# Kernel tuning notes

Hardware: AMD Instinct MI355X
Metric: run time of the kernel (lower is better)

## Reference

```python
import jax, jax.numpy as jnp
import numpy as np

BETA = 0.5
THRESHOLD = 14.0

def softplus_custom(x):
    # torch.nn.Softplus(beta=0.5, threshold=14): (1/beta)*log1p(exp(beta*x)) if beta*x<=threshold else x
    bx = BETA * x
    return jnp.where(bx > THRESHOLD, x, (1.0 / BETA) * jnp.log1p(jnp.exp(jnp.minimum(bx, THRESHOLD))))

def setup_inputs() -> dict:
    key = jax.random.key(0)
    ks = jax.random.split(key, 12)
    N, E, RBF, D = 50000, 800000, 100, 64
    inp = {
        'rbf': jax.random.normal(ks[0], (E, RBF), dtype=jnp.float32),
        'edge_f': jax.random.normal(ks[1], (E, D), dtype=jnp.float32),
        'new_node': jax.random.normal(ks[2], (N, D), dtype=jnp.float32),
        'W1': jax.random.normal(ks[3], (RBF, D), dtype=jnp.float32) * (1.0 / np.sqrt(RBF)),
        'b1': jax.random.normal(ks[4], (D,), dtype=jnp.float32) * 0.01,
        'W2': jax.random.normal(ks[5], (D, D), dtype=jnp.float32) * (1.0 / np.sqrt(D)),
        'b2': jax.random.normal(ks[6], (D,), dtype=jnp.float32) * 0.01,
        'W3': jax.random.normal(ks[7], (D, D), dtype=jnp.float32) * (1.0 / np.sqrt(D)),
        'b3': jax.random.normal(ks[8], (D,), dtype=jnp.float32) * 0.01,
        'src': jax.random.randint(ks[9], (E,), 0, N, dtype=jnp.int32),
        'dst': jax.random.randint(ks[10], (E,), 0, N, dtype=jnp.int32),
    }
    return inp

def reference(rbf, edge_f, new_node, W1, b1, W2, b2, W3, b3, src, dst):
    N = new_node.shape[0]
    # update_rbf: linear -> softplus(beta=0.5, threshold=14) -> linear, per edge
    h = softplus_custom(rbf @ W1 + b1) @ W2 + b2            # [E, D]
    # update_edge: linear on edge features
    edge_f_new = edge_f @ W3 + b3                            # [E, D]
    # message: u_mul_e (source node feature * edge h) and copy_e; reduce: segmented sum to dst
    msg = new_node[src] * h + edge_f_new                     # [E, D]
    out = jax.ops.segment_sum(msg, dst, num_segments=N)      # [N, D]
    return out
```

## Files before the change

kernel.cpp:

```cpp
#include <hip/hip_runtime.h>

#define RBF_DIM 100

typedef __attribute__((ext_vector_type(8))) short bf16x8;
typedef __attribute__((ext_vector_type(4))) float f32x4;

__device__ __forceinline__ unsigned short f2bf_sw(float f) {
    union { float f; unsigned int u; } v; v.f = f;
    unsigned int r = (v.u + 0x7FFFu + ((v.u >> 16) & 1u)) >> 16;
    return (unsigned short)r;
}

__device__ __forceinline__ unsigned int cvtpk(float x, float y) {
    unsigned int r;
    asm("v_cvt_pk_bf16_f32 %0, %1, %2" : "=v"(r) : "v"(x), "v"(y));
    return r;
}
__device__ __forceinline__ bf16x8 cvt8(f32x4 a, f32x4 b) {
    union { bf16x8 v; unsigned int u[4]; } r;
    r.u[0] = cvtpk(a[0], a[1]);
    r.u[1] = cvtpk(a[2], a[3]);
    r.u[2] = cvtpk(b[0], b[1]);
    r.u[3] = cvtpk(b[2], b[3]);
    return r.v;
}

__global__ void prep_weights(const float* __restrict__ W1, const float* __restrict__ b1,
                             const float* __restrict__ W2, const float* __restrict__ W3,
                             unsigned short* __restrict__ ws) {
    for (int e = threadIdx.x; e < 32 * 64 * 8; e += 256) {
        int f = e >> 9;
        int lane = (e >> 3) & 63;
        int j = e & 7;
        int l15 = lane & 15, g = lane >> 4;
        float v;
        if (f < 16) {
            int t4 = f >> 2, ks = f & 3;
            int k = 32 * ks + 8 * g + j, o = 16 * t4 + l15;
            v = (k < RBF_DIM) ? W1[k * 64 + o] : ((k == RBF_DIM) ? b1[o] : 0.0f);
        } else if (f < 24) {
            int q = f - 16, t4 = q >> 1, ks = q & 1;
            int k = 32 * ks + 8 * g + j, o = 16 * t4 + l15;
            v = W2[k * 64 + o];
        } else {
            int q = f - 24, t4 = q >> 1, ks = q & 1;
            int k = 32 * ks + 8 * g + j, o = 16 * t4 + l15;
            v = W3[k * 64 + o];
        }
        ws[e] = f2bf_sw(v);
    }
}

__global__ __launch_bounds__(512, 4)
void veconv_main(const float* __restrict__ rbf, const float* __restrict__ edge_f,
                 const float* __restrict__ node,
                 const float* __restrict__ b2, const float* __restrict__ b3,
                 const int* __restrict__ src, const int* __restrict__ dst,
                 const unsigned short* __restrict__ wsw,
                 float* __restrict__ out) {
    __shared__ unsigned short wlds[32 * 512];
    __shared__ unsigned short sp_lds[8 * 16 * 64];

    const int tid = threadIdx.x;
    const int lane = tid & 63, wid = tid >> 6;
    const int l15 = lane & 15, g = lane >> 4;
    const int ew0 = blockIdx.x * 128 + wid * 16;
    const int eg = ew0 + l15;
    const int swz = (l15 & 7) << 3;

    const float* rrow = rbf + (long)eg * RBF_DIM;
    const f32x4 ra0 = *(const f32x4*)(rrow + 8 * g);
    const f32x4 ra1 = *(const f32x4*)(rrow + 8 * g + 4);
    const f32x4 rb0 = *(const f32x4*)(rrow + 32 + 8 * g);
    const f32x4 rb1 = *(const f32x4*)(rrow + 32 + 8 * g + 4);
    const f32x4 rc0 = *(const f32x4*)(rrow + 64 + 8 * g);
    const f32x4 rc1 = *(const f32x4*)(rrow + 64 + 8 * g + 4);
    f32x4 rt = (f32x4){0.f, 0.f, 0.f, 0.f};
    if (g == 0) rt = *(const f32x4*)(rrow + 96);
    const float* erow = edge_f + (long)eg * 64;
    const f32x4 ea0 = *(const f32x4*)(erow + 8 * g);
    const f32x4 ea1 = *(const f32x4*)(erow + 8 * g + 4);
    const f32x4 eb0 = *(const f32x4*)(erow + 32 + 8 * g);
    const f32x4 eb1 = *(const f32x4*)(erow + 32 + 8 * g + 4);
    const int4 s4 = *(const int4*)(src + ew0 + 4 * g);
    const int4 d4 = *(const int4*)(dst + ew0 + 4 * g);
    float b2v[4], b3v[4];
#pragma unroll
    for (int t4 = 0; t4 < 4; ++t4) { b2v[t4] = b2[16 * t4 + l15]; b3v[t4] = b3[16 * t4 + l15]; }

    {
        const uint4* wg = (const uint4*)wsw;
        uint4* wl = (uint4*)wlds;
#pragma unroll
        for (int i = 0; i < 4; ++i) wl[tid + 512 * i] = wg[tid + 512 * i];
    }

    const int sv[4] = {s4.x, s4.y, s4.z, s4.w};
    const int dv[4] = {d4.x, d4.y, d4.z, d4.w};
    float nd[4][4];
#pragma unroll
    for (int r = 0; r < 4; ++r)
#pragma unroll
        for (int t4 = 0; t4 < 4; ++t4)
            nd[r][t4] = node[(long)sv[r] * 64 + 16 * t4 + l15];

    __syncthreads();

    const bf16x8* frg = (const bf16x8*)wlds;

    bf16x8 bfk[4];
    bfk[0] = cvt8(ra0, ra1);
    bfk[1] = cvt8(rb0, rb1);
    bfk[2] = cvt8(rc0, rc1);
    {
        union { bf16x8 v; unsigned int u[4]; } bt;
        bt.u[0] = (g == 0) ? cvtpk(rt[0], rt[1]) : 0u;
        bt.u[1] = (g == 0) ? cvtpk(rt[2], rt[3]) : 0u;
        bt.u[2] = (g == 0) ? 0x3F80u : 0u;
        bt.u[3] = 0u;
        bfk[3] = bt.v;
    }
    f32x4 acc1[4];
#pragma unroll
    for (int t4 = 0; t4 < 4; ++t4) acc1[t4] = (f32x4){0.f, 0.f, 0.f, 0.f};
#pragma unroll
    for (int ks = 0; ks < 4; ++ks)
#pragma unroll
        for (int t4 = 0; t4 < 4; ++t4)
            acc1[t4] = __builtin_amdgcn_mfma_f32_16x16x32_bf16(frg[(t4 * 4 + ks) * 64 + lane],
                                                               bfk[ks], acc1[t4], 0, 0, 0);

#pragma unroll
    for (int t4 = 0; t4 < 4; ++t4) {
        float spv[4];
#pragma unroll
        for (int r = 0; r < 4; ++r) {
            float x = acc1[t4][r];
            float bx = 0.5f * x;
            float s = 2.0f * __logf(1.0f + __expf(bx));
            spv[r] = (bx > 14.0f) ? x : s;
        }
        unsigned int p0 = cvtpk(spv[0], spv[1]);
        unsigned int p1 = cvtpk(spv[2], spv[3]);
        int el = (wid * 16 + l15) * 64 + ((16 * t4 + 4 * g) ^ swz);
        *(uint2*)&sp_lds[el] = make_uint2(p0, p1);
    }

    bf16x8 aef[2];
    aef[0] = cvt8(ea0, ea1);
    aef[1] = cvt8(eb0, eb1);
    f32x4 acc2[4], acc3[4];
#pragma unroll
    for (int t4 = 0; t4 < 4; ++t4) {
        acc2[t4] = (f32x4){0.f, 0.f, 0.f, 0.f};
        acc3[t4] = (f32x4){0.f, 0.f, 0.f, 0.f};
    }
#pragma unroll
    for (int ks = 0; ks < 2; ++ks) {
        bf16x8 asp = *(const bf16x8*)&sp_lds[(wid * 16 + l15) * 64 + ((32 * ks + 8 * g) ^ swz)];
#pragma unroll
        for (int t4 = 0; t4 < 4; ++t4) {
            acc2[t4] = __builtin_amdgcn_mfma_f32_16x16x32_bf16(asp,
                          frg[(16 + t4 * 2 + ks) * 64 + lane], acc2[t4], 0, 0, 0);
            acc3[t4] = __builtin_amdgcn_mfma_f32_16x16x32_bf16(aef[ks],
                          frg[(24 + t4 * 2 + ks) * 64 + lane], acc3[t4], 0, 0, 0);
        }
    }

#pragma unroll
    for (int r = 0; r < 4; ++r) {
        float* orow = out + (long)dv[r] * 64 + l15;
#pragma unroll
        for (int t4 = 0; t4 < 4; ++t4) {
            float msg = nd[r][t4] * (acc2[t4][r] + b2v[t4]) + (acc3[t4][r] + b3v[t4]);
            atomicAdd(&orow[16 * t4], msg);
        }
    }
}

extern "C" void kernel_launch(void* const* d_in, const int* in_sizes, int n_in,
                              void* d_out, int out_size, void* d_ws, size_t ws_size,
                              hipStream_t stream) {
    const float* rbf    = (const float*)d_in[0];
    const float* edge_f = (const float*)d_in[1];
    const float* node   = (const float*)d_in[2];
    const float* W1     = (const float*)d_in[3];
    const float* b1     = (const float*)d_in[4];
    const float* W2     = (const float*)d_in[5];
    const float* b2     = (const float*)d_in[6];
    const float* W3     = (const float*)d_in[7];
    const float* b3     = (const float*)d_in[8];
    const int*   src    = (const int*)d_in[9];
    const int*   dst    = (const int*)d_in[10];
    float* out = (float*)d_out;
    unsigned short* ws = (unsigned short*)d_ws;

    const int E = in_sizes[9];

    hipMemsetAsync(d_out, 0, (size_t)out_size * sizeof(float), stream);
    prep_weights<<<1, 256, 0, stream>>>(W1, b1, W2, W3, ws);
    veconv_main<<<E / 128, 512, 0, stream>>>(rbf, edge_f, node, b2, b3, src, dst, ws, out);
}
```

Baseline: 223.8 us.

## Replace float atomics with CSR bucketing of bf16 messages and segmented sum

Builds a CSR index over destination nodes using a histogram and a two-level scan. The main kernel then writes each edge message as bf16 into a slot reserved with one integer atomic per edge, and a separate kernel sums each node's messages without atomics. This is meant to remove the 64 float atomicAdds per edge on scattered destinations. In exchange it adds several small kernels, about 100MB of extra message traffic, and bf16 rounding of messages before summation, which costs accuracy. A fallback to the old atomic path remains if the workspace is too small.

New measurement: 250.8 us. +12.1%, slower.

```diff
diff --git a/kernel.cpp b/kernel.cpp
--- a/kernel.cpp
+++ b/kernel.cpp
@@ -10,7 +10,10 @@
     unsigned int r = (v.u + 0x7FFFu + ((v.u >> 16) & 1u)) >> 16;
     return (unsigned short)r;
 }
-
+__device__ __forceinline__ float bf2f(unsigned short u) {
+    union { unsigned int u; float f; } v; v.u = ((unsigned int)u) << 16;
+    return v.f;
+}
 __device__ __forceinline__ unsigned int cvtpk(float x, float y) {
     unsigned int r;
     asm("v_cvt_pk_bf16_f32 %0, %1, %2" : "=v"(r) : "v"(x), "v"(y));
@@ -51,13 +54,68 @@
     }
 }
 
+__global__ void k_hist(const int* __restrict__ dst, int* __restrict__ counts, int E) {
+    int i = blockIdx.x * 256 + threadIdx.x;
+    if (i < E) atomicAdd(&counts[dst[i]], 1);
+}
+
+__global__ void k_bsum(const int* __restrict__ counts, int* __restrict__ bsum, int N) {
+    __shared__ int red[4];
+    int i = blockIdx.x * 256 + threadIdx.x;
+    int v = (i < N) ? counts[i] : 0;
+    for (int off = 32; off; off >>= 1) v += __shfl_down(v, off, 64);
+    int lane = threadIdx.x & 63, w = threadIdx.x >> 6;
+    if (lane == 0) red[w] = v;
+    __syncthreads();
+    if (threadIdx.x == 0) bsum[blockIdx.x] = red[0] + red[1] + red[2] + red[3];
+}
+
+__global__ void k_scan_bsum(int* __restrict__ bsum, int* __restrict__ offs,
+                            int NB, int N, int E) {
+    __shared__ int s[256];
+    int t = threadIdx.x;
+    int v = (t < NB) ? bsum[t] : 0;
+    s[t] = v;
+    __syncthreads();
+    for (int off = 1; off < 256; off <<= 1) {
+        int x = (t >= off) ? s[t - off] : 0;
+        __syncthreads();
+        s[t] += x;
+        __syncthreads();
+    }
+    if (t < NB) bsum[t] = s[t] - v;
+    if (t == 0) offs[N] = E;
+}
+
+__global__ void k_scan_final(const int* __restrict__ counts, const int* __restrict__ bsum,
+                             int* __restrict__ offs, int* __restrict__ cursor, int N) {
+    __shared__ int s[256];
+    int t = threadIdx.x, i = blockIdx.x * 256 + t;
+    int v = (i < N) ? counts[i] : 0;
+    s[t] = v;
+    __syncthreads();
+    for (int off = 1; off < 256; off <<= 1) {
+        int x = (t >= off) ? s[t - off] : 0;
+        __syncthreads();
+        s[t] += x;
+        __syncthreads();
+    }
+    if (i < N) {
+        int excl = s[t] - v + bsum[blockIdx.x];
+        offs[i] = excl;
+        cursor[i] = excl;
+    }
+}
+
+template <bool CSR>
 __global__ __launch_bounds__(512, 4)
 void veconv_main(const float* __restrict__ rbf, const float* __restrict__ edge_f,
                  const float* __restrict__ node,
                  const float* __restrict__ b2, const float* __restrict__ b3,
                  const int* __restrict__ src, const int* __restrict__ dst,
                  const unsigned short* __restrict__ wsw,
-                 float* __restrict__ out) {
+                 float* __restrict__ out,
+                 unsigned short* __restrict__ msg, int* __restrict__ cursor) {
     __shared__ unsigned short wlds[32 * 512];
     __shared__ unsigned short sp_lds[8 * 16 * 64];
 
@@ -167,15 +225,53 @@
         }
     }
 
-#pragma unroll
-    for (int r = 0; r < 4; ++r) {
-        float* orow = out + (long)dv[r] * 64 + l15;
-#pragma unroll
-        for (int t4 = 0; t4 < 4; ++t4) {
-            float msg = nd[r][t4] * (acc2[t4][r] + b2v[t4]) + (acc3[t4][r] + b3v[t4]);
-            atomicAdd(&orow[16 * t4], msg);
-        }
-    }
+    if constexpr (CSR) {
+        int slot[4];
+#pragma unroll
+        for (int r = 0; r < 4; ++r) {
+            int sl = 0;
+            if (l15 == 0) sl = atomicAdd(&cursor[dv[r]], 1);
+            slot[r] = __shfl(sl, lane & 48, 64);
+        }
+#pragma unroll
+        for (int r = 0; r < 4; ++r) {
+            float m0 = nd[r][0] * (acc2[0][r] + b2v[0]) + (acc3[0][r] + b3v[0]);
+            float m1 = nd[r][1] * (acc2[1][r] + b2v[1]) + (acc3[1][r] + b3v[1]);
+            float m2 = nd[r][2] * (acc2[2][r] + b2v[2]) + (acc3[2][r] + b3v[2]);
+            float m3 = nd[r][3] * (acc2[3][r] + b2v[3]) + (acc3[3][r] + b3v[3]);
+            *(uint2*)(msg + (long)slot[r] * 64 + 4 * l15) =
+                make_uint2(cvtpk(m0, m1), cvtpk(m2, m3));
+        }
+    } else {
+#pragma unroll
+        for (int r = 0; r < 4; ++r) {
+            float* orow = out + (long)dv[r] * 64 + l15;
+#pragma unroll
+            for (int t4 = 0; t4 < 4; ++t4) {
+                float m = nd[r][t4] * (acc2[t4][r] + b2v[t4]) + (acc3[t4][r] + b3v[t4]);
+                atomicAdd(&orow[16 * t4], m);
+            }
+        }
+    }
+}
+
+__global__ __launch_bounds__(256)
+void k_segsum(const unsigned short* __restrict__ msg, const int* __restrict__ offs,
+              float* __restrict__ out, int N) {
+    int wid = threadIdx.x >> 6, lane = threadIdx.x & 63;
+    int n = blockIdx.x * 4 + wid;
+    if (n >= N) return;
+    int beg = offs[n], end = offs[n + 1];
+    float s0 = 0.f, s1 = 0.f, s2 = 0.f, s3 = 0.f;
+    int i = beg;
+    for (; i + 4 <= end; i += 4) {
+        s0 += bf2f(msg[(long)(i + 0) * 64 + lane]);
+        s1 += bf2f(msg[(long)(i + 1) * 64 + lane]);
+        s2 += bf2f(msg[(long)(i + 2) * 64 + lane]);
+        s3 += bf2f(msg[(long)(i + 3) * 64 + lane]);
+    }
+    for (; i < end; ++i) s0 += bf2f(msg[(long)i * 64 + lane]);
+    out[(long)n * 64 + 16 * (lane & 3) + (lane >> 2)] = s0 + s1 + s2 + s3;
 }
 
 extern "C" void kernel_launch(void* const* d_in, const int* in_sizes, int n_in,
@@ -193,11 +289,43 @@
     const int*   src    = (const int*)d_in[9];
     const int*   dst    = (const int*)d_in[10];
     float* out = (float*)d_out;
-    unsigned short* ws = (unsigned short*)d_ws;
+    char* ws = (char*)d_ws;
 
     const int E = in_sizes[9];
-
-    hipMemsetAsync(d_out, 0, (size_t)out_size * sizeof(float), stream);
-    prep_weights<<<1, 256, 0, stream>>>(W1, b1, W2, W3, ws);
-    veconv_main<<<E / 128, 512, 0, stream>>>(rbf, edge_f, node, b2, b3, src, dst, ws, out);
-}
+    const int N = in_sizes[2] / 64;
+    const int NB = (N + 255) / 256;
+
+    size_t off = 32768;
+    size_t counts_off = off; off += (size_t)N * 4;
+    size_t cursor_off = off; off += (size_t)N * 4;
+    size_t offs_off   = off; off += ((size_t)N + 1) * 4;
+    off = (off + 255) & ~(size_t)255;
+    size_t bsum_off = off; off += (size_t)NB * 4;
+    off = (off + 255) & ~(size_t)255;
+    size_t msg_off = off; off += (size_t)E * 64 * 2;
+    const bool use_csr = (NB <= 256) && (ws_size >= off);
+
+    unsigned short* wsw = (unsigned short*)(ws);
+    int* counts         = (int*)(ws + counts_off);
+    int* cursor         = (int*)(ws + cursor_off);
+    int* offs           = (int*)(ws + offs_off);
+    int* bsum           = (int*)(ws + bsum_off);
+    unsigned short* msg = (unsigned short*)(ws + msg_off);
+
+    prep_weights<<<1, 256, 0, stream>>>(W1, b1, W2, W3, wsw);
+
+    if (use_csr) {
+        hipMemsetAsync(counts, 0, (size_t)N * 4, stream);
+        k_hist<<<(E + 255) / 256, 256, 0, stream>>>(dst, counts, E);
+        k_bsum<<<NB, 256, 0, stream>>>(counts, bsum, N);
+        k_scan_bsum<<<1, 256, 0, stream>>>(bsum, offs, NB, N, E);
+        k_scan_final<<<NB, 256, 0, stream>>>(counts, bsum, offs, cursor, N);
+        veconv_main<true><<<E / 128, 512, 0, stream>>>(rbf, edge_f, node, b2, b3, src, dst,
+                                                       wsw, out, msg, cursor);
+        k_segsum<<<(N + 3) / 4, 256, 0, stream>>>(msg, offs, out, N);
+    } else {
+        hipMemsetAsync(out, 0, (size_t)out_size * sizeof(float), stream);
+        veconv_main<false><<<E / 128, 512, 0, stream>>>(rbf, edge_f, node, b2, b3, src, dst,
+                                                        wsw, out, msg, cursor);
+    }
+}
```

## Process two 16-edge tiles per wave to amortize weight LDS staging

Applied to the files above, without the earlier changes.

Each wave now handles 32 edges (two 16-edge sub-tiles) instead of 16, so each block covers 256 edges and the grid is halved. All rbf and edge_f loads for both sub-tiles are issued before the barrier to raise memory-level parallelism. The per-block copy of the bf16 weights into LDS is amortized over twice as many edges. In exchange, register pressure rises from holding both tiles' inputs, which may cut occupancy under the launch bound of 512 threads and 4 blocks, and there are fewer blocks to fill the GPU.

Result: slower. 254.8 us (+13.9%).

```diff
diff --git a/kernel.cpp b/kernel.cpp
--- a/kernel.cpp
+++ b/kernel.cpp
@@ -10,7 +10,6 @@
     unsigned int r = (v.u + 0x7FFFu + ((v.u >> 16) & 1u)) >> 16;
     return (unsigned short)r;
 }
-
 __device__ __forceinline__ unsigned int cvtpk(float x, float y) {
     unsigned int r;
     asm("v_cvt_pk_bf16_f32 %0, %1, %2" : "=v"(r) : "v"(x), "v"(y));
@@ -59,34 +58,51 @@
                  const unsigned short* __restrict__ wsw,
                  float* __restrict__ out) {
     __shared__ unsigned short wlds[32 * 512];
-    __shared__ unsigned short sp_lds[8 * 16 * 64];
+    __shared__ unsigned short sp_lds[8 * 32 * 64];
 
     const int tid = threadIdx.x;
     const int lane = tid & 63, wid = tid >> 6;
     const int l15 = lane & 15, g = lane >> 4;
-    const int ew0 = blockIdx.x * 128 + wid * 16;
-    const int eg = ew0 + l15;
+    const int ewA = blockIdx.x * 256 + wid * 32;
+    const int ewB = ewA + 16;
+    const int egA = ewA + l15, egB = ewB + l15;
     const int swz = (l15 & 7) << 3;
 
-    const float* rrow = rbf + (long)eg * RBF_DIM;
-    const f32x4 ra0 = *(const f32x4*)(rrow + 8 * g);
-    const f32x4 ra1 = *(const f32x4*)(rrow + 8 * g + 4);
-    const f32x4 rb0 = *(const f32x4*)(rrow + 32 + 8 * g);
-    const f32x4 rb1 = *(const f32x4*)(rrow + 32 + 8 * g + 4);
-    const f32x4 rc0 = *(const f32x4*)(rrow + 64 + 8 * g);
-    const f32x4 rc1 = *(const f32x4*)(rrow + 64 + 8 * g + 4);
-    f32x4 rt = (f32x4){0.f, 0.f, 0.f, 0.f};
-    if (g == 0) rt = *(const f32x4*)(rrow + 96);
-    const float* erow = edge_f + (long)eg * 64;
-    const f32x4 ea0 = *(const f32x4*)(erow + 8 * g);
-    const f32x4 ea1 = *(const f32x4*)(erow + 8 * g + 4);
-    const f32x4 eb0 = *(const f32x4*)(erow + 32 + 8 * g);
-    const f32x4 eb1 = *(const f32x4*)(erow + 32 + 8 * g + 4);
-    const int4 s4 = *(const int4*)(src + ew0 + 4 * g);
-    const int4 d4 = *(const int4*)(dst + ew0 + 4 * g);
-    float b2v[4], b3v[4];
-#pragma unroll
-    for (int t4 = 0; t4 < 4; ++t4) { b2v[t4] = b2[16 * t4 + l15]; b3v[t4] = b3[16 * t4 + l15]; }
+    const int4 s4A = *(const int4*)(src + ewA + 4 * g);
+    const int4 d4A = *(const int4*)(dst + ewA + 4 * g);
+    const int4 s4B = *(const int4*)(src + ewB + 4 * g);
+    const int4 d4B = *(const int4*)(dst + ewB + 4 * g);
+
+    const float* rrA = rbf + (long)egA * RBF_DIM;
+    const f32x4 rA0 = *(const f32x4*)(rrA + 8 * g);
+    const f32x4 rA1 = *(const f32x4*)(rrA + 8 * g + 4);
+    const f32x4 rA2 = *(const f32x4*)(rrA + 32 + 8 * g);
+    const f32x4 rA3 = *(const f32x4*)(rrA + 32 + 8 * g + 4);
+    const f32x4 rA4 = *(const f32x4*)(rrA + 64 + 8 * g);
+    const f32x4 rA5 = *(const f32x4*)(rrA + 64 + 8 * g + 4);
+    f32x4 rtA = (f32x4){0.f, 0.f, 0.f, 0.f};
+    if (g == 0) rtA = *(const f32x4*)(rrA + 96);
+
+    const float* rrB = rbf + (long)egB * RBF_DIM;
+    const f32x4 rB0 = *(const f32x4*)(rrB + 8 * g);
+    const f32x4 rB1 = *(const f32x4*)(rrB + 8 * g + 4);
+    const f32x4 rB2 = *(const f32x4*)(rrB + 32 + 8 * g);
+    const f32x4 rB3 = *(const f32x4*)(rrB + 32 + 8 * g + 4);
+    const f32x4 rB4 = *(const f32x4*)(rrB + 64 + 8 * g);
+    const f32x4 rB5 = *(const f32x4*)(rrB + 64 + 8 * g + 4);
+    f32x4 rtB = (f32x4){0.f, 0.f, 0.f, 0.f};
+    if (g == 0) rtB = *(const f32x4*)(rrB + 96);
+
+    const float* erA = edge_f + (long)egA * 64;
+    const f32x4 eA0 = *(const f32x4*)(erA + 8 * g);
+    const f32x4 eA1 = *(const f32x4*)(erA + 8 * g + 4);
+    const f32x4 eA2 = *(const f32x4*)(erA + 32 + 8 * g);
+    const f32x4 eA3 = *(const f32x4*)(erA + 32 + 8 * g + 4);
+    const float* erB = edge_f + (long)egB * 64;
+    const f32x4 eB0 = *(const f32x4*)(erB + 8 * g);
+    const f32x4 eB1 = *(const f32x4*)(erB + 8 * g + 4);
+    const f32x4 eB2 = *(const f32x4*)(erB + 32 + 8 * g);
+    const f32x4 eB3 = *(const f32x4*)(erB + 32 + 8 * g + 4);
 
     {
         const uint4* wg = (const uint4*)wsw;
@@ -94,86 +110,101 @@
 #pragma unroll
         for (int i = 0; i < 4; ++i) wl[tid + 512 * i] = wg[tid + 512 * i];
     }
-
-    const int sv[4] = {s4.x, s4.y, s4.z, s4.w};
-    const int dv[4] = {d4.x, d4.y, d4.z, d4.w};
-    float nd[4][4];
-#pragma unroll
-    for (int r = 0; r < 4; ++r)
-#pragma unroll
-        for (int t4 = 0; t4 < 4; ++t4)
-            nd[r][t4] = node[(long)sv[r] * 64 + 16 * t4 + l15];
-
-    __syncthreads();
-
-    const bf16x8* frg = (const bf16x8*)wlds;
-
-    bf16x8 bfk[4];
-    bfk[0] = cvt8(ra0, ra1);
-    bfk[1] = cvt8(rb0, rb1);
-    bfk[2] = cvt8(rc0, rc1);
+    float b2v[4], b3v[4];
+#pragma unroll
+    for (int t4 = 0; t4 < 4; ++t4) { b2v[t4] = b2[16 * t4 + l15]; b3v[t4] = b3[16 * t4 + l15]; }
+
+    bf16x8 bfkA[4], bfkB[4], aeA[2], aeB[2];
+    bfkA[0] = cvt8(rA0, rA1); bfkA[1] = cvt8(rA2, rA3); bfkA[2] = cvt8(rA4, rA5);
+    bfkB[0] = cvt8(rB0, rB1); bfkB[1] = cvt8(rB2, rB3); bfkB[2] = cvt8(rB4, rB5);
     {
         union { bf16x8 v; unsigned int u[4]; } bt;
-        bt.u[0] = (g == 0) ? cvtpk(rt[0], rt[1]) : 0u;
-        bt.u[1] = (g == 0) ? cvtpk(rt[2], rt[3]) : 0u;
+        bt.u[0] = (g == 0) ? cvtpk(rtA[0], rtA[1]) : 0u;
+        bt.u[1] = (g == 0) ? cvtpk(rtA[2], rtA[3]) : 0u;
         bt.u[2] = (g == 0) ? 0x3F80u : 0u;
         bt.u[3] = 0u;
-        bfk[3] = bt.v;
-    }
-    f32x4 acc1[4];
-#pragma unroll
-    for (int t4 = 0; t4 < 4; ++t4) acc1[t4] = (f32x4){0.f, 0.f, 0.f, 0.f};
-#pragma unroll
-    for (int ks = 0; ks < 4; ++ks)
-#pragma unroll
-        for (int t4 = 0; t4 < 4; ++t4)
-            acc1[t4] = __builtin_amdgcn_mfma_f32_16x16x32_bf16(frg[(t4 * 4 + ks) * 64 + lane],
-                                                               bfk[ks], acc1[t4], 0, 0, 0);
-
-#pragma unroll
-    for (int t4 = 0; t4 < 4; ++t4) {
-        float spv[4];
+        bfkA[3] = bt.v;
+        bt.u[0] = (g == 0) ? cvtpk(rtB[0], rtB[1]) : 0u;
+        bt.u[1] = (g == 0) ? cvtpk(rtB[2], rtB[3]) : 0u;
+        bt.u[2] = (g == 0) ? 0x3F80u : 0u;
+        bt.u[3] = 0u;
+        bfkB[3] = bt.v;
+    }
+    aeA[0] = cvt8(eA0, eA1); aeA[1] = cvt8(eA2, eA3);
+    aeB[0] = cvt8(eB0, eB1); aeB[1] = cvt8(eB2, eB3);
+
+    __syncthreads();
+
+    const bf16x8* frg = (const bf16x8*)wlds;
+
+#pragma unroll
+    for (int sub = 0; sub < 2; ++sub) {
+        const bf16x8* bfk = (sub == 0) ? bfkA : bfkB;
+        const bf16x8* ae  = (sub == 0) ? aeA  : aeB;
+        const int4 s4 = (sub == 0) ? s4A : s4B;
+        const int4 d4 = (sub == 0) ? d4A : d4B;
+        unsigned short* spb = sp_lds + (wid * 32 + sub * 16) * 64;
+
+        const int sv[4] = {s4.x, s4.y, s4.z, s4.w};
+        const int dv[4] = {d4.x, d4.y, d4.z, d4.w};
+        float nd[4][4];
+#pragma unroll
+        for (int r = 0; r < 4; ++r)
+#pragma unroll
+            for (int t4 = 0; t4 < 4; ++t4)
+                nd[r][t4] = node[(long)sv[r] * 64 + 16 * t4 + l15];
+
+        f32x4 acc1[4];
+#pragma unroll
+        for (int t4 = 0; t4 < 4; ++t4) acc1[t4] = (f32x4){0.f, 0.f, 0.f, 0.f};
+#pragma unroll
+        for (int ks = 0; ks < 4; ++ks)
+#pragma unroll
+            for (int t4 = 0; t4 < 4; ++t4)
+                acc1[t4] = __builtin_amdgcn_mfma_f32_16x16x32_bf16(
+                    frg[(t4 * 4 + ks) * 64 + lane], bfk[ks], acc1[t4], 0, 0, 0);
+
+#pragma unroll
+        for (int t4 = 0; t4 < 4; ++t4) {
+            float spv[4];
+#pragma unroll
+            for (int r = 0; r < 4; ++r) {
+                float x = acc1[t4][r];
+                float bx = 0.5f * x;
+                float s = 2.0f * __logf(1.0f + __expf(bx));
+                spv[r] = (bx > 14.0f) ? x : s;
+            }
+            unsigned int p0 = cvtpk(spv[0], spv[1]);
+            unsigned int p1 = cvtpk(spv[2], spv[3]);
+            *(uint2*)&spb[l15 * 64 + ((16 * t4 + 4 * g) ^ swz)] = make_uint2(p0, p1);
+        }
+
+        f32x4 acc2[4], acc3[4];
+#pragma unroll
+        for (int t4 = 0; t4 < 4; ++t4) {
+            acc2[t4] = (f32x4){0.f, 0.f, 0.f, 0.f};
+            acc3[t4] = (f32x4){0.f, 0.f, 0.f, 0.f};
+        }
+#pragma unroll
+        for (int ks = 0; ks < 2; ++ks) {
+            bf16x8 asp = *(const bf16x8*)&spb[l15 * 64 + ((32 * ks + 8 * g) ^ swz)];
+#pragma unroll
+            for (int t4 = 0; t4 < 4; ++t4) {
+                acc2[t4] = __builtin_amdgcn_mfma_f32_16x16x32_bf16(asp,
+                              frg[(16 + t4 * 2 + ks) * 64 + lane], acc2[t4], 0, 0, 0);
+                acc3[t4] = __builtin_amdgcn_mfma_f32_16x16x32_bf16(ae[ks],
+                              frg[(24 + t4 * 2 + ks) * 64 + lane], acc3[t4], 0, 0, 0);
+            }
+        }
+
 #pragma unroll
         for (int r = 0; r < 4; ++r) {
-            float x = acc1[t4][r];
-            float bx = 0.5f * x;
-            float s = 2.0f * __logf(1.0f + __expf(bx));
-            spv[r] = (bx > 14.0f) ? x : s;
-        }
-        unsigned int p0 = cvtpk(spv[0], spv[1]);
-        unsigned int p1 = cvtpk(spv[2], spv[3]);
-        int el = (wid * 16 + l15) * 64 + ((16 * t4 + 4 * g) ^ swz);
-        *(uint2*)&sp_lds[el] = make_uint2(p0, p1);
-    }
-
-    bf16x8 aef[2];
-    aef[0] = cvt8(ea0, ea1);
-    aef[1] = cvt8(eb0, eb1);
-    f32x4 acc2[4], acc3[4];
-#pragma unroll
-    for (int t4 = 0; t4 < 4; ++t4) {
-        acc2[t4] = (f32x4){0.f, 0.f, 0.f, 0.f};
-        acc3[t4] = (f32x4){0.f, 0.f, 0.f, 0.f};
-    }
-#pragma unroll
-    for (int ks = 0; ks < 2; ++ks) {
-        bf16x8 asp = *(const bf16x8*)&sp_lds[(wid * 16 + l15) * 64 + ((32 * ks + 8 * g) ^ swz)];
-#pragma unroll
-        for (int t4 = 0; t4 < 4; ++t4) {
-            acc2[t4] = __builtin_amdgcn_mfma_f32_16x16x32_bf16(asp,
-                          frg[(16 + t4 * 2 + ks) * 64 + lane], acc2[t4], 0, 0, 0);
-            acc3[t4] = __builtin_amdgcn_mfma_f32_16x16x32_bf16(aef[ks],
-                          frg[(24 + t4 * 2 + ks) * 64 + lane], acc3[t4], 0, 0, 0);
-        }
-    }
-
-#pragma unroll
-    for (int r = 0; r < 4; ++r) {
-        float* orow = out + (long)dv[r] * 64 + l15;
-#pragma unroll
-        for (int t4 = 0; t4 < 4; ++t4) {
-            float msg = nd[r][t4] * (acc2[t4][r] + b2v[t4]) + (acc3[t4][r] + b3v[t4]);
-            atomicAdd(&orow[16 * t4], msg);
+            float* orow = out + (long)dv[r] * 64 + l15;
+#pragma unroll
+            for (int t4 = 0; t4 < 4; ++t4) {
+                float msg = nd[r][t4] * (acc2[t4][r] + b2v[t4]) + (acc3[t4][r] + b3v[t4]);
+                atomicAdd(&orow[16 * t4], msg);
+            }
         }
     }
 }
@@ -197,7 +228,7 @@
 
     const int E = in_sizes[9];
 
-    hipMemsetAsync(d_out, 0, (size_t)out_size * sizeof(float), stream);
+    (void)hipMemsetAsync(d_out, 0, (size_t)out_size * sizeof(float), stream);
     prep_weights<<<1, 256, 0, stream>>>(W1, b1, W2, W3, ws);
-    veconv_main<<<E / 128, 512, 0, stream>>>(rbf, edge_f, node, b2, b3, src, dst, ws, out);
-}
+    veconv_main<<<E / 256, 512, 0, stream>>>(rbf, edge_f, node, b2, b3, src, dst, ws, out);
+}
```

## Make blocks persistent over several tiles with double-buffered async rbf loads into LDS

Applied to the files above, without the earlier changes.

Each block now processes up to five 128-edge tiles instead of one. It loads the weight fragments into LDS once per block rather than once per tile. The rbf rows for the next tile are prefetched into a double-buffered LDS region with global_load_lds DMA while the current tile computes. The extra 100KB of LDS limits occupancy to fewer blocks per CU, launch bounds drop to 2, and a __syncthreads per tile is added.

After: 230.6 us. 1.03x slower.

```diff
diff --git a/kernel.cpp b/kernel.cpp
--- a/kernel.cpp
+++ b/kernel.cpp
@@ -1,6 +1,7 @@
 #include <hip/hip_runtime.h>
 
 #define RBF_DIM 100
+#define NT 5
 
 typedef __attribute__((ext_vector_type(8))) short bf16x8;
 typedef __attribute__((ext_vector_type(4))) float f32x4;
@@ -10,7 +11,6 @@
     unsigned int r = (v.u + 0x7FFFu + ((v.u >> 16) & 1u)) >> 16;
     return (unsigned short)r;
 }
-
 __device__ __forceinline__ unsigned int cvtpk(float x, float y) {
     unsigned int r;
     asm("v_cvt_pk_bf16_f32 %0, %1, %2" : "=v"(r) : "v"(x), "v"(y));
@@ -23,6 +23,10 @@
     r.u[2] = cvtpk(b[0], b[1]);
     r.u[3] = cvtpk(b[2], b[3]);
     return r.v;
+}
+__device__ __forceinline__ void dma16(const float* g, void* l) {
+    __builtin_amdgcn_global_load_lds((const __attribute__((address_space(1))) void*)g,
+                                     (__attribute__((address_space(3))) void*)l, 16, 0, 0);
 }
 
 __global__ void prep_weights(const float* __restrict__ W1, const float* __restrict__ b1,
@@ -51,42 +55,22 @@
     }
 }
 
-__global__ __launch_bounds__(512, 4)
+__global__ __launch_bounds__(512, 2)
 void veconv_main(const float* __restrict__ rbf, const float* __restrict__ edge_f,
                  const float* __restrict__ node,
                  const float* __restrict__ b2, const float* __restrict__ b3,
                  const int* __restrict__ src, const int* __restrict__ dst,
                  const unsigned short* __restrict__ wsw,
-                 float* __restrict__ out) {
+                 float* __restrict__ out, int ntiles) {
     __shared__ unsigned short wlds[32 * 512];
+    __shared__ float rbuf[2][128 * 100];
     __shared__ unsigned short sp_lds[8 * 16 * 64];
 
     const int tid = threadIdx.x;
     const int lane = tid & 63, wid = tid >> 6;
     const int l15 = lane & 15, g = lane >> 4;
-    const int ew0 = blockIdx.x * 128 + wid * 16;
-    const int eg = ew0 + l15;
     const int swz = (l15 & 7) << 3;
-
-    const float* rrow = rbf + (long)eg * RBF_DIM;
-    const f32x4 ra0 = *(const f32x4*)(rrow + 8 * g);
-    const f32x4 ra1 = *(const f32x4*)(rrow + 8 * g + 4);
-    const f32x4 rb0 = *(const f32x4*)(rrow + 32 + 8 * g);
-    const f32x4 rb1 = *(const f32x4*)(rrow + 32 + 8 * g + 4);
-    const f32x4 rc0 = *(const f32x4*)(rrow + 64 + 8 * g);
-    const f32x4 rc1 = *(const f32x4*)(rrow + 64 + 8 * g + 4);
-    f32x4 rt = (f32x4){0.f, 0.f, 0.f, 0.f};
-    if (g == 0) rt = *(const f32x4*)(rrow + 96);
-    const float* erow = edge_f + (long)eg * 64;
-    const f32x4 ea0 = *(const f32x4*)(erow + 8 * g);
-    const f32x4 ea1 = *(const f32x4*)(erow + 8 * g + 4);
-    const f32x4 eb0 = *(const f32x4*)(erow + 32 + 8 * g);
-    const f32x4 eb1 = *(const f32x4*)(erow + 32 + 8 * g + 4);
-    const int4 s4 = *(const int4*)(src + ew0 + 4 * g);
-    const int4 d4 = *(const int4*)(dst + ew0 + 4 * g);
-    float b2v[4], b3v[4];
-#pragma unroll
-    for (int t4 = 0; t4 < 4; ++t4) { b2v[t4] = b2[16 * t4 + l15]; b3v[t4] = b3[16 * t4 + l15]; }
+    const long tile0 = (long)blockIdx.x * NT;
 
     {
         const uint4* wg = (const uint4*)wsw;
@@ -94,87 +78,123 @@
 #pragma unroll
         for (int i = 0; i < 4; ++i) wl[tid + 512 * i] = wg[tid + 512 * i];
     }
-
-    const int sv[4] = {s4.x, s4.y, s4.z, s4.w};
-    const int dv[4] = {d4.x, d4.y, d4.z, d4.w};
-    float nd[4][4];
-#pragma unroll
-    for (int r = 0; r < 4; ++r)
-#pragma unroll
-        for (int t4 = 0; t4 < 4; ++t4)
-            nd[r][t4] = node[(long)sv[r] * 64 + 16 * t4 + l15];
-
+    float b2v[4], b3v[4];
+#pragma unroll
+    for (int t4 = 0; t4 < 4; ++t4) { b2v[t4] = b2[16 * t4 + l15]; b3v[t4] = b3[16 * t4 + l15]; }
+
+    {
+        const float* gt = rbf + tile0 * 128 * RBF_DIM;
+        for (int c = wid; c < 50; c += 8)
+            dma16(gt + c * 256 + lane * 4, (char*)&rbuf[0][0] + c * 1024);
+    }
     __syncthreads();
 
     const bf16x8* frg = (const bf16x8*)wlds;
 
-    bf16x8 bfk[4];
-    bfk[0] = cvt8(ra0, ra1);
-    bfk[1] = cvt8(rb0, rb1);
-    bfk[2] = cvt8(rc0, rc1);
-    {
-        union { bf16x8 v; unsigned int u[4]; } bt;
-        bt.u[0] = (g == 0) ? cvtpk(rt[0], rt[1]) : 0u;
-        bt.u[1] = (g == 0) ? cvtpk(rt[2], rt[3]) : 0u;
-        bt.u[2] = (g == 0) ? 0x3F80u : 0u;
-        bt.u[3] = 0u;
-        bfk[3] = bt.v;
-    }
-    f32x4 acc1[4];
-#pragma unroll
-    for (int t4 = 0; t4 < 4; ++t4) acc1[t4] = (f32x4){0.f, 0.f, 0.f, 0.f};
-#pragma unroll
-    for (int ks = 0; ks < 4; ++ks)
-#pragma unroll
-        for (int t4 = 0; t4 < 4; ++t4)
-            acc1[t4] = __builtin_amdgcn_mfma_f32_16x16x32_bf16(frg[(t4 * 4 + ks) * 64 + lane],
-                                                               bfk[ks], acc1[t4], 0, 0, 0);
-
-#pragma unroll
-    for (int t4 = 0; t4 < 4; ++t4) {
-        float spv[4];
+    for (int i = 0; i < NT; ++i) {
+        const long tile = tile0 + i;
+        if (tile >= ntiles) break;
+        const int cur = i & 1;
+
+        if (i + 1 < NT && tile + 1 < ntiles) {
+            const float* gt = rbf + (tile + 1) * 128 * RBF_DIM;
+            for (int c = wid; c < 50; c += 8)
+                dma16(gt + c * 256 + lane * 4, (char*)&rbuf[cur ^ 1][0] + c * 1024);
+        }
+
+        const int ew0 = (int)(tile * 128) + wid * 16;
+        const int eg = ew0 + l15;
+        const int4 s4 = *(const int4*)(src + ew0 + 4 * g);
+        const int4 d4 = *(const int4*)(dst + ew0 + 4 * g);
+        const float* erow = edge_f + (long)eg * 64;
+        const f32x4 ea0 = *(const f32x4*)(erow + 8 * g);
+        const f32x4 ea1 = *(const f32x4*)(erow + 8 * g + 4);
+        const f32x4 eb0 = *(const f32x4*)(erow + 32 + 8 * g);
+        const f32x4 eb1 = *(const f32x4*)(erow + 32 + 8 * g + 4);
+        const int sv[4] = {s4.x, s4.y, s4.z, s4.w};
+        const int dv[4] = {d4.x, d4.y, d4.z, d4.w};
+        float nd[4][4];
+#pragma unroll
+        for (int r = 0; r < 4; ++r)
+#pragma unroll
+            for (int t4 = 0; t4 < 4; ++t4)
+                nd[r][t4] = node[(long)sv[r] * 64 + 16 * t4 + l15];
+
+        const float* rrow = &rbuf[cur][(wid * 16 + l15) * RBF_DIM];
+        bf16x8 bfk[4];
+#pragma unroll
+        for (int ks = 0; ks < 3; ++ks) {
+            f32x4 a = *(const f32x4*)(rrow + 32 * ks + 8 * g);
+            f32x4 b = *(const f32x4*)(rrow + 32 * ks + 8 * g + 4);
+            bfk[ks] = cvt8(a, b);
+        }
+        {
+            f32x4 t = (g == 0) ? *(const f32x4*)(rrow + 96) : (f32x4){0.f, 0.f, 0.f, 0.f};
+            union { bf16x8 v; unsigned int u[4]; } bt;
+            bt.u[0] = (g == 0) ? cvtpk(t[0], t[1]) : 0u;
+            bt.u[1] = (g == 0) ? cvtpk(t[2], t[3]) : 0u;
+            bt.u[2] = (g == 0) ? 0x3F80u : 0u;
+            bt.u[3] = 0u;
+            bfk[3] = bt.v;
+        }
+        f32x4 acc1[4];
+#pragma unroll
+        for (int t4 = 0; t4 < 4; ++t4) acc1[t4] = (f32x4){0.f, 0.f, 0.f, 0.f};
+#pragma unroll
+        for (int ks = 0; ks < 4; ++ks)
+#pragma unroll
+            for (int t4 = 0; t4 < 4; ++t4)
+                acc1[t4] = __builtin_amdgcn_mfma_f32_16x16x32_bf16(
+                    frg[(t4 * 4 + ks) * 64 + lane], bfk[ks], acc1[t4], 0, 0, 0);
+
+#pragma unroll
+        for (int t4 = 0; t4 < 4; ++t4) {
+            float spv[4];
+#pragma unroll
+            for (int r = 0; r < 4; ++r) {
+                float x = acc1[t4][r];
+                float bx = 0.5f * x;
+                float s = 2.0f * __logf(1.0f + __expf(bx));
+                spv[r] = (bx > 14.0f) ? x : s;
+            }
+            unsigned int p0 = cvtpk(spv[0], spv[1]);
+            unsigned int p1 = cvtpk(spv[2], spv[3]);
+            int el = (wid * 16 + l15) * 64 + ((16 * t4 + 4 * g) ^ swz);
+            *(uint2*)&sp_lds[el] = make_uint2(p0, p1);
+        }
+
+        bf16x8 aef[2];
+        aef[0] = cvt8(ea0, ea1);
+        aef[1] = cvt8(eb0, eb1);
+        f32x4 acc2[4], acc3[4];
+#pragma unroll
+        for (int t4 = 0; t4 < 4; ++t4) {
+            acc2[t4] = (f32x4){0.f, 0.f, 0.f, 0.f};
+            acc3[t4] = (f32x4){0.f, 0.f, 0.f, 0.f};
+        }
+#pragma unroll
+        for (int ks = 0; ks < 2; ++ks) {
+            bf16x8 asp = *(const bf16x8*)&sp_lds[(wid * 16 + l15) * 64 + ((32 * ks + 8 * g) ^ swz)];
+#pragma unroll
+            for (int t4 = 0; t4 < 4; ++t4) {
+                acc2[t4] = __builtin_amdgcn_mfma_f32_16x16x32_bf16(asp,
+                              frg[(16 + t4 * 2 + ks) * 64 + lane], acc2[t4], 0, 0, 0);
+                acc3[t4] = __builtin_amdgcn_mfma_f32_16x16x32_bf16(aef[ks],
+                              frg[(24 + t4 * 2 + ks) * 64 + lane], acc3[t4], 0, 0, 0);
+            }
+        }
+
 #pragma unroll
         for (int r = 0; r < 4; ++r) {
-            float x = acc1[t4][r];
-            float bx = 0.5f * x;
-            float s = 2.0f * __logf(1.0f + __expf(bx));
-            spv[r] = (bx > 14.0f) ? x : s;
-        }
-        unsigned int p0 = cvtpk(spv[0], spv[1]);
-        unsigned int p1 = cvtpk(spv[2], spv[3]);
-        int el = (wid * 16 + l15) * 64 + ((16 * t4 + 4 * g) ^ swz);
-        *(uint2*)&sp_lds[el] = make_uint2(p0, p1);
-    }
-
-    bf16x8 aef[2];
-    aef[0] = cvt8(ea0, ea1);
-    aef[1] = cvt8(eb0, eb1);
-    f32x4 acc2[4], acc3[4];
-#pragma unroll
-    for (int t4 = 0; t4 < 4; ++t4) {
-        acc2[t4] = (f32x4){0.f, 0.f, 0.f, 0.f};
-        acc3[t4] = (f32x4){0.f, 0.f, 0.f, 0.f};
-    }
-#pragma unroll
-    for (int ks = 0; ks < 2; ++ks) {
-        bf16x8 asp = *(const bf16x8*)&sp_lds[(wid * 16 + l15) * 64 + ((32 * ks + 8 * g) ^ swz)];
-#pragma unroll
-        for (int t4 = 0; t4 < 4; ++t4) {
-            acc2[t4] = __builtin_amdgcn_mfma_f32_16x16x32_bf16(asp,
-                          frg[(16 + t4 * 2 + ks) * 64 + lane], acc2[t4], 0, 0, 0);
-            acc3[t4] = __builtin_amdgcn_mfma_f32_16x16x32_bf16(aef[ks],
-                          frg[(24 + t4 * 2 + ks) * 64 + lane], acc3[t4], 0, 0, 0);
-        }
-    }
-
-#pragma unroll
-    for (int r = 0; r < 4; ++r) {
-        float* orow = out + (long)dv[r] * 64 + l15;
-#pragma unroll
-        for (int t4 = 0; t4 < 4; ++t4) {
-            float msg = nd[r][t4] * (acc2[t4][r] + b2v[t4]) + (acc3[t4][r] + b3v[t4]);
-            atomicAdd(&orow[16 * t4], msg);
-        }
+            float* orow = out + (long)dv[r] * 64 + l15;
+#pragma unroll
+            for (int t4 = 0; t4 < 4; ++t4) {
+                float msg = nd[r][t4] * (acc2[t4][r] + b2v[t4]) + (acc3[t4][r] + b3v[t4]);
+                atomicAdd(&orow[16 * t4], msg);
+            }
+        }
+
+        __syncthreads();
     }
 }
 
@@ -196,8 +216,10 @@
     unsigned short* ws = (unsigned short*)d_ws;
 
     const int E = in_sizes[9];
-
-    hipMemsetAsync(d_out, 0, (size_t)out_size * sizeof(float), stream);
+    const int ntiles = E / 128;
+    const int grid = (ntiles + NT - 1) / NT;
+
+    (void)hipMemsetAsync(d_out, 0, (size_t)out_size * sizeof(float), stream);
     prep_weights<<<1, 256, 0, stream>>>(W1, b1, W2, W3, ws);
-    veconv_main<<<E / 128, 512, 0, stream>>>(rbf, edge_f, node, b2, b3, src, dst, ws, out);
-}
+    veconv_main<<<grid, 512, 0, stream>>>(rbf, edge_f, node, b2, b3, src, dst, ws, out, ntiles);
+}
```
